# Performance work log

Measured on AMD Instinct MI355X. Metric: run time of the kernel, lower is better.

## Reference

```python
import jax, jax.numpy as jnp
import numpy as np

# Dimensions: batch B, window W (time features), nodes M, hidden HID, hops NLAYERS
B, W, M, HID, NLAYERS = 32, 168, 2048, 128, 6


def setup_inputs() -> dict:
    key = jax.random.key(0)
    ks = jax.random.split(key, 6)
    x = jax.random.normal(ks[0], (B, W, M), dtype=jnp.float32)
    # scale L so matrix powers L^k stay bounded (spectral radius < 1)
    L = jax.random.normal(ks[1], (M, M), dtype=jnp.float32) / (2.0 * np.float32(np.sqrt(M)))
    # stacked per-hop MLP params: linears[i]: W->HID, linears2[i]: HID->1
    W1 = jax.random.normal(ks[2], (NLAYERS + 1, HID, W), dtype=jnp.float32) / np.float32(np.sqrt(W))
    b1 = jax.random.normal(ks[3], (NLAYERS + 1, HID), dtype=jnp.float32) * 0.01
    W2 = jax.random.normal(ks[4], (NLAYERS + 1, HID), dtype=jnp.float32) / np.float32(np.sqrt(HID))
    b2 = jax.random.normal(ks[5], (NLAYERS + 1,), dtype=jnp.float32) * 0.01
    return {"x": x, "L": L, "W1": W1, "b1": b1, "W2": W2, "b2": b2}


def _hop_mlp(t, w1, bb1, w2, bb2):
    # t: [B, M, W] -> scalar score per node: Linear(W->HID), ReLU, Linear(HID->1)
    h = jax.nn.relu(jnp.einsum('bmw,hw->bmh', t, w1) + bb1)
    return jnp.einsum('bmh,h->bm', h, w2) + bb2


def reference(x, L, W1, b1, W2, b2):
    xt = jnp.swapaxes(x, 1, 2)  # [B, M, W] (x.transpose(2,1))
    s = _hop_mlp(xt, W1[0], b1[0], W2[0], b2[0])  # [B, M]
    P = L
    for i in range(1, NLAYERS + 1):
        # PP.expand + bmm == broadcasted matmul; never materialize [B,M,M]
        t = jnp.einsum('ij,bjw->biw', P, xt)  # [B, M, W]
        s = s + _hop_mlp(t, W1[i], b1[i], W2[i], b2[i])
        P = jnp.matmul(L, P)  # next graph power
    return s  # [B, M]; output_fun is None so no final nonlinearity
```

## Files before the change

kernel.cpp:

```cpp
#include <hip/hip_runtime.h>
#include <cstdint>
#include <cstddef>

typedef __bf16 bf16_t;
typedef __attribute__((ext_vector_type(8))) __bf16 bf16x8;
typedef __attribute__((ext_vector_type(4))) __bf16 bf16x4;
typedef __attribute__((ext_vector_type(4))) float floatx4;

#define NB 32
#define NW 168
#define NM 2048
#define NHID 128
#define NBW (NB * NW)
#define NGEMM 168
#define NMLPB 256

#define GLOAD_LDS16(g, l)                                          \
  __builtin_amdgcn_global_load_lds(                                \
      (const __attribute__((address_space(1))) void*)(g),          \
      (__attribute__((address_space(3))) void*)(l), 16, 0, 0)

__global__ void cast_bf16_kernel(const float* __restrict__ in, bf16_t* __restrict__ out, int n4) {
  int stride = gridDim.x * blockDim.x;
  for (int i = blockIdx.x * blockDim.x + threadIdx.x; i < n4; i += stride) {
    float4 v = ((const float4*)in)[i];
    bf16x4 o = {(bf16_t)v.x, (bf16_t)v.y, (bf16_t)v.z, (bf16_t)v.w};
    ((bf16x4*)out)[i] = o;
  }
}

__global__ void prep_x_kernel(const float* __restrict__ x, bf16_t* __restrict__ Xb,
                              bf16_t* __restrict__ XT) {
  __shared__ float tile[64][65];
  const int R = NBW, C = NM;
  int r0 = blockIdx.y * 64, c0 = blockIdx.x * 64;
  int t = threadIdx.x;
  int tr = t >> 4, tc4 = (t & 15) * 4;
#pragma unroll
  for (int p = 0; p < 4; ++p) {
    int row = p * 16 + tr;
    float4 v = *(const float4*)(x + (size_t)(r0 + row) * C + c0 + tc4);
    tile[row][tc4 + 0] = v.x;
    tile[row][tc4 + 1] = v.y;
    tile[row][tc4 + 2] = v.z;
    tile[row][tc4 + 3] = v.w;
    bf16x4 o = {(bf16_t)v.x, (bf16_t)v.y, (bf16_t)v.z, (bf16_t)v.w};
    *(bf16x4*)(Xb + (size_t)(r0 + row) * C + c0 + tc4) = o;
  }
  __syncthreads();
#pragma unroll
  for (int p = 0; p < 4; ++p) {
    int c = p * 16 + tr;
    bf16x4 o = {(bf16_t)tile[tc4 + 0][c], (bf16_t)tile[tc4 + 1][c],
                (bf16_t)tile[tc4 + 2][c], (bf16_t)tile[tc4 + 3][c]};
    *(bf16x4*)(XT + (size_t)(c0 + c) * R + r0 + tc4) = o;
  }
}

__device__ __forceinline__ void mlp_half(
    int t2, int r0, bf16_t* __restrict__ Bs, float* __restrict__ sred,
    const bf16_t* __restrict__ T, const bf16_t* __restrict__ Wh,
    const float* __restrict__ b1h, const float* __restrict__ w2h, float b2v,
    float* __restrict__ out, int accumulate) {
  int lane = t2 & 63, wvh = t2 >> 6;
  int wm = wvh >> 1, wn = wvh & 1;
  int quad = lane >> 4, l15 = lane & 15;

  for (int c = 2688 + t2; c < 3072; c += 256) {
    int4 z = {0, 0, 0, 0};
    *(int4*)(Bs + (size_t)c * 8) = z;
  }
  for (int i = 0; i < 11; ++i) {
    int c = i * 256 + t2;
    if (c < 2688) {
      int kc = c >> 7;
      int h = (c & 127) ^ ((kc & 3) << 2);
      GLOAD_LDS16(Wh + (size_t)h * NW + kc * 8, Bs + (size_t)(i * 256 + wvh * 64) * 8);
    }
  }

  const bf16_t* arow[4];
#pragma unroll
  for (int mi = 0; mi < 4; ++mi) {
    int R = r0 + wm * 64 + mi * 16 + l15;
    arow[mi] = T + (size_t)(R >> 5) * NBW + (size_t)(R & 31) * NW + quad * 8;
  }

  floatx4 zero4 = {0.f, 0.f, 0.f, 0.f};
  floatx4 acc[4][4];
#pragma unroll
  for (int mi = 0; mi < 4; ++mi)
#pragma unroll
    for (int ni = 0; ni < 4; ++ni) acc[mi][ni] = zero4;

  __syncthreads();

#pragma unroll
  for (int kb = 0; kb < 192; kb += 32) {
    int kc = (kb >> 3) + quad;
    bf16x8 af[4], bf[4];
#pragma unroll
    for (int mi = 0; mi < 4; ++mi)
      af[mi] = *(const bf16x8*)(arow[mi] + kb);
#pragma unroll
    for (int ni = 0; ni < 4; ++ni) {
      int hpos = (wn * 64 + ni * 16 + l15) ^ ((kc & 3) << 2);
      bf[ni] = *(const bf16x8*)(Bs + (size_t)(kc * 128 + hpos) * 8);
    }
#pragma unroll
    for (int mi = 0; mi < 4; ++mi)
#pragma unroll
      for (int ni = 0; ni < 4; ++ni)
        acc[mi][ni] = __builtin_amdgcn_mfma_f32_16x16x32_bf16(af[mi], bf[ni], acc[mi][ni], 0, 0, 0);
  }

  float part[4][4];
#pragma unroll
  for (int mi = 0; mi < 4; ++mi)
#pragma unroll
    for (int r = 0; r < 4; ++r) part[mi][r] = 0.f;
#pragma unroll
  for (int ni = 0; ni < 4; ++ni) {
    int col = wn * 64 + ni * 16 + l15;
    float b1v = b1h[col];
    float w2v = w2h[col];
#pragma unroll
    for (int mi = 0; mi < 4; ++mi)
#pragma unroll
      for (int r = 0; r < 4; ++r) {
        float h = acc[mi][ni][r] + b1v;
        h = h > 0.f ? h : 0.f;
        part[mi][r] += h * w2v;
      }
  }
#pragma unroll
  for (int off = 1; off < 16; off <<= 1)
#pragma unroll
    for (int mi = 0; mi < 4; ++mi)
#pragma unroll
      for (int r = 0; r < 4; ++r) part[mi][r] += __shfl_xor(part[mi][r], off);
  if (l15 == 0) {
#pragma unroll
    for (int mi = 0; mi < 4; ++mi)
#pragma unroll
      for (int r = 0; r < 4; ++r) sred[wvh * 64 + mi * 16 + quad * 4 + r] = part[mi][r];
  }
  __syncthreads();
  if (t2 < 128) {
    int hh = t2 >> 6;
    int lr = t2 & 63;
    float v = sred[(hh * 2) * 64 + lr] + sred[(hh * 2 + 1) * 64 + lr] + b2v;
    int R = r0 + hh * 64 + lr;
    int idx = (R & 31) * NM + (R >> 5);
    if (accumulate)
      out[idx] += v;
    else
      out[idx] = v;
  }
}

#define STAGE2(gbase, ld, t, ks, ldsbase)                                        \
  do {                                                                           \
    const bf16_t* _g = (gbase) + (size_t)(t) * 64 + (ks) * 32;                   \
    GLOAD_LDS16(_g, lds + (ldsbase) + (ks) * 8192 + wv * 512);                   \
    GLOAD_LDS16(_g + (size_t)128 * (ld),                                         \
                lds + (ldsbase) + (ks) * 8192 + 4096 + wv * 512);                \
  } while (0)

#define VM4 asm volatile("s_waitcnt vmcnt(4)" ::: "memory")

#define PHASE(bufoff, ks, mh, READB, STG, WAIT)                                  \
  do {                                                                           \
    if (READB) {                                                                 \
      _Pragma("unroll") for (int ni = 0; ni < 4; ++ni)                           \
          bfr[ni] = *(const bf16x8*)(pB + (bufoff) + (ks) * 8192 + ni * 512);    \
    }                                                                            \
    _Pragma("unroll") for (int mi = 0; mi < 4; ++mi)                             \
        afr[mi] =                                                                \
            *(const bf16x8*)(pA + (bufoff) + (ks) * 8192 + ((mh) * 4 + mi) * 512); \
    __builtin_amdgcn_s_barrier();                                                \
    asm volatile("s_waitcnt lgkmcnt(0)" ::: "memory");                           \
    __builtin_amdgcn_s_setprio(1);                                               \
    _Pragma("unroll") for (int mi = 0; mi < 4; ++mi)                             \
        _Pragma("unroll") for (int ni = 0; ni < 4; ++ni)                         \
            acc[(mh) * 4 + mi][ni] = __builtin_amdgcn_mfma_f32_16x16x32_bf16(    \
                afr[mi], bfr[ni], acc[(mh) * 4 + mi][ni], 0, 0, 0);              \
    __builtin_amdgcn_s_setprio(0);                                               \
    STG;                                                                         \
    WAIT;                                                                        \
    __builtin_amdgcn_s_barrier();                                                \
  } while (0)

__global__ __launch_bounds__(512, 2) void fused_gemm_mlp_kernel(
    const bf16_t* __restrict__ A, const bf16_t* __restrict__ Bt,
    bf16_t* __restrict__ C, bf16_t* __restrict__ Ct,
    int K, int lda, int ldb, int ldc, int ldct, int write_c,
    const bf16_t* __restrict__ T, const bf16_t* __restrict__ W1b,
    const float* __restrict__ b1, const float* __restrict__ W2,
    const float* __restrict__ b2, float* __restrict__ out,
    int hop, int accumulate) {
  __shared__ bf16_t lds[65536];
  const int bx = blockIdx.x;
  const int tid = threadIdx.x;

  if (bx >= NGEMM) {
    int j = bx - NGEMM;
    int h = tid >> 8;
    int t2 = tid & 255;
    bf16_t* Bs = lds + (size_t)h * 24576;
    float* sred = (float*)(lds + 49152) + h * 256;
    int r0 = (2 * j + h) * 128;
    mlp_half(t2, r0, Bs, sred, T, W1b + (size_t)hop * NHID * NW,
             b1 + hop * NHID, W2 + hop * NHID, b2[hop], out, accumulate);
    return;
  }

  const int m0 = (bx >> 3) * 256, n0 = (bx & 7) * 256;
  const int lane = tid & 63, wv = tid >> 6;
  const int wm = wv >> 2, wn = wv & 3;
  const int quad = lane >> 4, l15 = lane & 15;

  const int srow = tid >> 2;
  const int scsw = (tid & 3) ^ ((srow >> 1) & 3);
  const bf16_t* aS = A + (size_t)(m0 + srow) * lda + scsw * 8;
  const bf16_t* bS = Bt + (size_t)(n0 + srow) * ldb + scsw * 8;

  const int fsw = (quad ^ ((l15 >> 1) & 3)) * 8;
  const bf16_t* pA = lds + (size_t)(wm * 128 + l15) * 32 + fsw;
  const bf16_t* pB = lds + 16384 + (size_t)(wn * 64 + l15) * 32 + fsw;

  floatx4 zero4 = {0.f, 0.f, 0.f, 0.f};
  floatx4 acc[8][4];
#pragma unroll
  for (int mi = 0; mi < 8; ++mi)
#pragma unroll
    for (int ni = 0; ni < 4; ++ni) acc[mi][ni] = zero4;

  STAGE2(aS, lda, 0, 0, 0);
  STAGE2(bS, ldb, 0, 0, 16384);
  STAGE2(aS, lda, 0, 1, 0);
  STAGE2(bS, ldb, 0, 1, 16384);
  STAGE2(aS, lda, 1, 0, 32768);
  STAGE2(bS, ldb, 1, 0, 49152);
  VM4;
  __builtin_amdgcn_s_barrier();

  bf16x8 afr[4], bfr[4];
  const int nt = K >> 6;
  const int nit = K >> 7;
#pragma unroll 1
  for (int i = 0; i < nit; ++i) {
    const int t1 = 2 * i + 1;
    const int t2 = (t1 + 1 < nt) ? t1 + 1 : 0;
    const int t3 = (t1 + 2 < nt) ? t1 + 2 : 0;
    PHASE(0,     0, 0, 1, STAGE2(aS, lda, t1, 1, 32768), (void)0);
    PHASE(0,     0, 1, 0, STAGE2(bS, ldb, t1, 1, 49152), (void)0);
    PHASE(0,     1, 0, 1, STAGE2(aS, lda, t2, 0, 0),     (void)0);
    PHASE(0,     1, 1, 0, STAGE2(bS, ldb, t2, 0, 16384), VM4);
    PHASE(32768, 0, 0, 1, STAGE2(aS, lda, t2, 1, 0),     (void)0);
    PHASE(32768, 0, 1, 0, STAGE2(bS, ldb, t2, 1, 16384), (void)0);
    PHASE(32768, 1, 0, 1, STAGE2(aS, lda, t3, 0, 32768), (void)0);
    PHASE(32768, 1, 1, 0, STAGE2(bS, ldb, t3, 0, 49152), VM4);
  }
  asm volatile("s_waitcnt vmcnt(0)" ::: "memory");

#pragma unroll
  for (int mi = 0; mi < 8; ++mi) {
#pragma unroll
    for (int ni = 0; ni < 4; ++ni) {
      int col = n0 + wn * 64 + ni * 16 + l15;
      int rowb = m0 + wm * 128 + mi * 16 + quad * 4;
      bf16x4 tv;
#pragma unroll
      for (int r = 0; r < 4; ++r) tv[r] = (bf16_t)acc[mi][ni][r];
      *(bf16x4*)(Ct + (size_t)col * ldct + rowb) = tv;
      if (write_c) {
#pragma unroll
        for (int r = 0; r < 4; ++r)
          C[(size_t)(rowb + r) * ldc + col] = tv[r];
      }
    }
  }
}

__global__ void mlp_score_kernel(const bf16_t* __restrict__ T, const bf16_t* __restrict__ W1b,
                                 const float* __restrict__ b1, const float* __restrict__ W2,
                                 const float* __restrict__ b2, float* __restrict__ out,
                                 int hop, int accumulate) {
  __shared__ bf16_t Bs[24 * 128 * 8];
  __shared__ float sred[256];
  mlp_half(threadIdx.x, blockIdx.x * 128, Bs, sred, T,
           W1b + (size_t)hop * NHID * NW, b1 + hop * NHID, W2 + hop * NHID,
           b2[hop], out, accumulate);
}

extern "C" void kernel_launch(void* const* d_in, const int* in_sizes, int n_in,
                              void* d_out, int out_size, void* d_ws, size_t ws_size,
                              hipStream_t stream) {
  const float* x = (const float*)d_in[0];
  const float* L = (const float*)d_in[1];
  const float* W1 = (const float*)d_in[2];
  const float* b1 = (const float*)d_in[3];
  const float* W2 = (const float*)d_in[4];
  const float* b2 = (const float*)d_in[5];
  float* out = (float*)d_out;

  char* ws = (char*)d_ws;
  size_t off = 0;
  auto walloc = [&](size_t bytes) -> void* {
    off = (off + 255) & ~(size_t)255;
    void* p = ws + off;
    off += bytes;
    return p;
  };
  bf16_t* Xb = (bf16_t*)walloc((size_t)NBW * NM * 2);
  bf16_t* XT0 = (bf16_t*)walloc((size_t)NM * NBW * 2);
  bf16_t* XT1 = (bf16_t*)walloc((size_t)NM * NBW * 2);
  bf16_t* Lb = (bf16_t*)walloc((size_t)NM * NM * 2);
  bf16_t* W1b = (bf16_t*)walloc((size_t)7 * NHID * NW * 2);
  bf16_t* Ta = (bf16_t*)walloc((size_t)NBW * NM * 2);
  (void)ws_size; (void)in_sizes; (void)n_in; (void)out_size;

  prep_x_kernel<<<dim3(NM / 64, NBW / 64), dim3(256), 0, stream>>>(x, Xb, XT0);
  cast_bf16_kernel<<<dim3(1024), dim3(256), 0, stream>>>(L, Lb, NM * NM / 4);
  cast_bf16_kernel<<<dim3(64), dim3(256), 0, stream>>>(W1, W1b, 7 * NHID * NW / 4);

  bf16_t* src = Xb;
  bf16_t* dst = Ta;
  bf16_t* xtprev = XT0;
  bf16_t* xtcur = XT1;
  for (int i = 1; i <= 6; ++i) {
    fused_gemm_mlp_kernel<<<dim3(NGEMM + NMLPB), dim3(512), 0, stream>>>(
        src, Lb, dst, xtcur, NM, NM, NM, NM, NBW, (i < 6) ? 1 : 0,
        xtprev, W1b, b1, W2, b2, out, i - 1, (i > 1) ? 1 : 0);
    bf16_t* t = src; src = dst; dst = t;
    t = xtprev; xtprev = xtcur; xtcur = t;
  }
  mlp_score_kernel<<<dim3(NM * NB / 128), dim3(256), 0, stream>>>(
      xtprev, W1b, b1, W2, b2, out, 6, 1);
}
```

Measured before the change: 473.6 us.

## Double-buffer LDS fragment reads in GEMM loop and split MLP blocks

The GEMM main loop now reads the next A/B fragments from LDS into a second register set before issuing the current MFMAs. This replaces the read-barrier-wait-compute phases with a software-pipelined schedule that has fewer full barriers and a looser vmcnt wait. The MLP side of the fused kernel changes from two 128-row halves per 512-thread block to one 128-row tile per block, doubling the MLP block count. In those blocks only 256 threads compute, which may waste occupancy, and the extra fragment registers add register pressure.

```diff
diff --git a/kernel.cpp b/kernel.cpp
--- a/kernel.cpp
+++ b/kernel.cpp
@@ -13,7 +13,7 @@
 #define NHID 128
 #define NBW (NB * NW)
 #define NGEMM 168
-#define NMLPB 256
+#define NMLPB 512
 
 #define GLOAD_LDS16(g, l)                                          \
   __builtin_amdgcn_global_load_lds(                                \
@@ -57,98 +57,99 @@
   }
 }
 
-__device__ __forceinline__ void mlp_half(
-    int t2, int r0, bf16_t* __restrict__ Bs, float* __restrict__ sred,
+__device__ __forceinline__ void mlp_single(
+    int tid, int r0, bf16_t* __restrict__ Bs,
     const bf16_t* __restrict__ T, const bf16_t* __restrict__ Wh,
     const float* __restrict__ b1h, const float* __restrict__ w2h, float b2v,
     float* __restrict__ out, int accumulate) {
-  int lane = t2 & 63, wvh = t2 >> 6;
-  int wm = wvh >> 1, wn = wvh & 1;
-  int quad = lane >> 4, l15 = lane & 15;
-
-  for (int c = 2688 + t2; c < 3072; c += 256) {
-    int4 z = {0, 0, 0, 0};
-    *(int4*)(Bs + (size_t)c * 8) = z;
-  }
-  for (int i = 0; i < 11; ++i) {
-    int c = i * 256 + t2;
-    if (c < 2688) {
+  float* sred = (float*)(Bs + 24576);
+  int lane = tid & 63, wv2 = tid >> 6;
+
+#pragma unroll
+  for (int i = 0; i < 6; ++i) {
+    int c = i * 512 + tid;
+    if (c >= 2688) {
+      int4 z = {0, 0, 0, 0};
+      *(int4*)(Bs + (size_t)c * 8) = z;
+    } else {
       int kc = c >> 7;
       int h = (c & 127) ^ ((kc & 3) << 2);
-      GLOAD_LDS16(Wh + (size_t)h * NW + kc * 8, Bs + (size_t)(i * 256 + wvh * 64) * 8);
-    }
-  }
-
-  const bf16_t* arow[4];
-#pragma unroll
-  for (int mi = 0; mi < 4; ++mi) {
-    int R = r0 + wm * 64 + mi * 16 + l15;
-    arow[mi] = T + (size_t)(R >> 5) * NBW + (size_t)(R & 31) * NW + quad * 8;
-  }
-
-  floatx4 zero4 = {0.f, 0.f, 0.f, 0.f};
-  floatx4 acc[4][4];
-#pragma unroll
-  for (int mi = 0; mi < 4; ++mi)
-#pragma unroll
-    for (int ni = 0; ni < 4; ++ni) acc[mi][ni] = zero4;
-
+      GLOAD_LDS16(Wh + (size_t)h * NW + kc * 8, Bs + (size_t)(i * 512 + wv2 * 64) * 8);
+    }
+  }
   __syncthreads();
 
-#pragma unroll
-  for (int kb = 0; kb < 192; kb += 32) {
-    int kc = (kb >> 3) + quad;
-    bf16x8 af[4], bf[4];
+  if (tid < 256) {
+    int wm = wv2 >> 1, wn = wv2 & 1;
+    int quad = lane >> 4, l15 = lane & 15;
+    const bf16_t* arow[4];
+#pragma unroll
+    for (int mi = 0; mi < 4; ++mi) {
+      int R = r0 + wm * 64 + mi * 16 + l15;
+      arow[mi] = T + (size_t)(R >> 5) * NBW + (size_t)(R & 31) * NW + quad * 8;
+    }
+    floatx4 zero4 = {0.f, 0.f, 0.f, 0.f};
+    floatx4 acc[4][4];
 #pragma unroll
     for (int mi = 0; mi < 4; ++mi)
-      af[mi] = *(const bf16x8*)(arow[mi] + kb);
+#pragma unroll
+      for (int ni = 0; ni < 4; ++ni) acc[mi][ni] = zero4;
+
+#pragma unroll
+    for (int kb = 0; kb < 192; kb += 32) {
+      int kc = (kb >> 3) + quad;
+      bf16x8 af[4], bf[4];
+#pragma unroll
+      for (int mi = 0; mi < 4; ++mi)
+        af[mi] = *(const bf16x8*)(arow[mi] + kb);
+#pragma unroll
+      for (int ni = 0; ni < 4; ++ni) {
+        int hpos = (wn * 64 + ni * 16 + l15) ^ ((kc & 3) << 2);
+        bf[ni] = *(const bf16x8*)(Bs + (size_t)(kc * 128 + hpos) * 8);
+      }
+#pragma unroll
+      for (int mi = 0; mi < 4; ++mi)
+#pragma unroll
+        for (int ni = 0; ni < 4; ++ni)
+          acc[mi][ni] = __builtin_amdgcn_mfma_f32_16x16x32_bf16(af[mi], bf[ni], acc[mi][ni], 0, 0, 0);
+    }
+
+    float part[4][4];
+#pragma unroll
+    for (int mi = 0; mi < 4; ++mi)
+#pragma unroll
+      for (int r = 0; r < 4; ++r) part[mi][r] = 0.f;
 #pragma unroll
     for (int ni = 0; ni < 4; ++ni) {
-      int hpos = (wn * 64 + ni * 16 + l15) ^ ((kc & 3) << 2);
-      bf[ni] = *(const bf16x8*)(Bs + (size_t)(kc * 128 + hpos) * 8);
-    }
-#pragma unroll
-    for (int mi = 0; mi < 4; ++mi)
-#pragma unroll
-      for (int ni = 0; ni < 4; ++ni)
-        acc[mi][ni] = __builtin_amdgcn_mfma_f32_16x16x32_bf16(af[mi], bf[ni], acc[mi][ni], 0, 0, 0);
-  }
-
-  float part[4][4];
-#pragma unroll
-  for (int mi = 0; mi < 4; ++mi)
-#pragma unroll
-    for (int r = 0; r < 4; ++r) part[mi][r] = 0.f;
-#pragma unroll
-  for (int ni = 0; ni < 4; ++ni) {
-    int col = wn * 64 + ni * 16 + l15;
-    float b1v = b1h[col];
-    float w2v = w2h[col];
-#pragma unroll
-    for (int mi = 0; mi < 4; ++mi)
-#pragma unroll
-      for (int r = 0; r < 4; ++r) {
-        float h = acc[mi][ni][r] + b1v;
-        h = h > 0.f ? h : 0.f;
-        part[mi][r] += h * w2v;
-      }
-  }
-#pragma unroll
-  for (int off = 1; off < 16; off <<= 1)
-#pragma unroll
-    for (int mi = 0; mi < 4; ++mi)
-#pragma unroll
-      for (int r = 0; r < 4; ++r) part[mi][r] += __shfl_xor(part[mi][r], off);
-  if (l15 == 0) {
-#pragma unroll
-    for (int mi = 0; mi < 4; ++mi)
-#pragma unroll
-      for (int r = 0; r < 4; ++r) sred[wvh * 64 + mi * 16 + quad * 4 + r] = part[mi][r];
+      int col = wn * 64 + ni * 16 + l15;
+      float b1v = b1h[col];
+      float w2v = w2h[col];
+#pragma unroll
+      for (int mi = 0; mi < 4; ++mi)
+#pragma unroll
+        for (int r = 0; r < 4; ++r) {
+          float h = acc[mi][ni][r] + b1v;
+          h = h > 0.f ? h : 0.f;
+          part[mi][r] += h * w2v;
+        }
+    }
+#pragma unroll
+    for (int off = 1; off < 16; off <<= 1)
+#pragma unroll
+      for (int mi = 0; mi < 4; ++mi)
+#pragma unroll
+        for (int r = 0; r < 4; ++r) part[mi][r] += __shfl_xor(part[mi][r], off);
+    if (l15 == 0) {
+#pragma unroll
+      for (int mi = 0; mi < 4; ++mi)
+#pragma unroll
+        for (int r = 0; r < 4; ++r) sred[wv2 * 64 + mi * 16 + quad * 4 + r] = part[mi][r];
+    }
   }
   __syncthreads();
-  if (t2 < 128) {
-    int hh = t2 >> 6;
-    int lr = t2 & 63;
+  if (tid < 128) {
+    int hh = tid >> 6;
+    int lr = tid & 63;
     float v = sred[(hh * 2) * 64 + lr] + sred[(hh * 2 + 1) * 64 + lr] + b2v;
     int R = r0 + hh * 64 + lr;
     int idx = (R & 31) * NM + (R >> 5);
@@ -167,28 +168,26 @@
                 lds + (ldsbase) + (ks) * 8192 + 4096 + wv * 512);                \
   } while (0)
 
-#define VM4 asm volatile("s_waitcnt vmcnt(4)" ::: "memory")
-
-#define PHASE(bufoff, ks, mh, READB, STG, WAIT)                                  \
+#define VM6 asm volatile("s_waitcnt vmcnt(6)" ::: "memory")
+#define TOPB asm volatile("s_barrier" ::: "memory")
+#define ENDB __builtin_amdgcn_s_barrier()
+
+#define RD_A(dst, bufoff, ks, mh)                                                \
+  _Pragma("unroll") for (int mi = 0; mi < 4; ++mi)                               \
+      dst[mi] = *(const bf16x8*)(pA + (bufoff) + (ks) * 8192 + ((mh) * 4 + mi) * 512)
+
+#define RD_B(dst, bufoff, ks)                                                    \
+  _Pragma("unroll") for (int ni = 0; ni < 4; ++ni)                               \
+      dst[ni] = *(const bf16x8*)(pB + (bufoff) + (ks) * 8192 + ni * 512)
+
+#define MM16(af_, bf_, mh)                                                       \
   do {                                                                           \
-    if (READB) {                                                                 \
-      _Pragma("unroll") for (int ni = 0; ni < 4; ++ni)                           \
-          bfr[ni] = *(const bf16x8*)(pB + (bufoff) + (ks) * 8192 + ni * 512);    \
-    }                                                                            \
-    _Pragma("unroll") for (int mi = 0; mi < 4; ++mi)                             \
-        afr[mi] =                                                                \
-            *(const bf16x8*)(pA + (bufoff) + (ks) * 8192 + ((mh) * 4 + mi) * 512); \
-    __builtin_amdgcn_s_barrier();                                                \
-    asm volatile("s_waitcnt lgkmcnt(0)" ::: "memory");                           \
     __builtin_amdgcn_s_setprio(1);                                               \
     _Pragma("unroll") for (int mi = 0; mi < 4; ++mi)                             \
         _Pragma("unroll") for (int ni = 0; ni < 4; ++ni)                         \
             acc[(mh) * 4 + mi][ni] = __builtin_amdgcn_mfma_f32_16x16x32_bf16(    \
-                afr[mi], bfr[ni], acc[(mh) * 4 + mi][ni], 0, 0, 0);              \
+                af_[mi], bf_[ni], acc[(mh) * 4 + mi][ni], 0, 0, 0);              \
     __builtin_amdgcn_s_setprio(0);                                               \
-    STG;                                                                         \
-    WAIT;                                                                        \
-    __builtin_amdgcn_s_barrier();                                                \
   } while (0)
 
 __global__ __launch_bounds__(512, 2) void fused_gemm_mlp_kernel(
@@ -205,13 +204,8 @@
 
   if (bx >= NGEMM) {
     int j = bx - NGEMM;
-    int h = tid >> 8;
-    int t2 = tid & 255;
-    bf16_t* Bs = lds + (size_t)h * 24576;
-    float* sred = (float*)(lds + 49152) + h * 256;
-    int r0 = (2 * j + h) * 128;
-    mlp_half(t2, r0, Bs, sred, T, W1b + (size_t)hop * NHID * NW,
-             b1 + hop * NHID, W2 + hop * NHID, b2[hop], out, accumulate);
+    mlp_single(tid, j * 128, lds, T, W1b + (size_t)hop * NHID * NW,
+               b1 + hop * NHID, W2 + hop * NHID, b2[hop], out, accumulate);
     return;
   }
 
@@ -242,10 +236,13 @@
   STAGE2(bS, ldb, 0, 1, 16384);
   STAGE2(aS, lda, 1, 0, 32768);
   STAGE2(bS, ldb, 1, 0, 49152);
-  VM4;
-  __builtin_amdgcn_s_barrier();
-
-  bf16x8 afr[4], bfr[4];
+  asm volatile("s_waitcnt vmcnt(8)" ::: "memory");
+  TOPB;
+
+  bf16x8 af0[4], af1[4], bf0[4], bf1[4];
+  RD_B(bf0, 0, 0);
+  RD_A(af0, 0, 0, 0);
+
   const int nt = K >> 6;
   const int nit = K >> 7;
 #pragma unroll 1
@@ -253,14 +250,46 @@
     const int t1 = 2 * i + 1;
     const int t2 = (t1 + 1 < nt) ? t1 + 1 : 0;
     const int t3 = (t1 + 2 < nt) ? t1 + 2 : 0;
-    PHASE(0,     0, 0, 1, STAGE2(aS, lda, t1, 1, 32768), (void)0);
-    PHASE(0,     0, 1, 0, STAGE2(bS, ldb, t1, 1, 49152), (void)0);
-    PHASE(0,     1, 0, 1, STAGE2(aS, lda, t2, 0, 0),     (void)0);
-    PHASE(0,     1, 1, 0, STAGE2(bS, ldb, t2, 0, 16384), VM4);
-    PHASE(32768, 0, 0, 1, STAGE2(aS, lda, t2, 1, 0),     (void)0);
-    PHASE(32768, 0, 1, 0, STAGE2(bS, ldb, t2, 1, 16384), (void)0);
-    PHASE(32768, 1, 0, 1, STAGE2(aS, lda, t3, 0, 32768), (void)0);
-    PHASE(32768, 1, 1, 0, STAGE2(bS, ldb, t3, 0, 49152), VM4);
+    RD_A(af1, 0, 0, 1);
+    MM16(af0, bf0, 0);
+    STAGE2(aS, lda, t1, 1, 32768);
+    ENDB;
+    VM6; TOPB;
+    RD_B(bf1, 0, 1);
+    RD_A(af0, 0, 1, 0);
+    MM16(af1, bf0, 1);
+    STAGE2(bS, ldb, t1, 1, 49152);
+    ENDB;
+    RD_A(af1, 0, 1, 1);
+    MM16(af0, bf1, 0);
+    STAGE2(aS, lda, t2, 0, 0);
+    ENDB;
+    VM6; TOPB;
+    RD_B(bf0, 32768, 0);
+    RD_A(af0, 32768, 0, 0);
+    MM16(af1, bf1, 1);
+    STAGE2(bS, ldb, t2, 0, 16384);
+    ENDB;
+    RD_A(af1, 32768, 0, 1);
+    MM16(af0, bf0, 0);
+    STAGE2(aS, lda, t2, 1, 0);
+    ENDB;
+    VM6; TOPB;
+    RD_B(bf1, 32768, 1);
+    RD_A(af0, 32768, 1, 0);
+    MM16(af1, bf0, 1);
+    STAGE2(bS, ldb, t2, 1, 16384);
+    ENDB;
+    RD_A(af1, 32768, 1, 1);
+    MM16(af0, bf1, 0);
+    STAGE2(aS, lda, t3, 0, 32768);
+    ENDB;
+    VM6; TOPB;
+    RD_B(bf0, 0, 0);
+    RD_A(af0, 0, 0, 0);
+    MM16(af1, bf1, 1);
+    STAGE2(bS, ldb, t3, 0, 49152);
+    ENDB;
   }
   asm volatile("s_waitcnt vmcnt(0)" ::: "memory");
 
@@ -283,15 +312,15 @@
   }
 }
 
-__global__ void mlp_score_kernel(const bf16_t* __restrict__ T, const bf16_t* __restrict__ W1b,
-                                 const float* __restrict__ b1, const float* __restrict__ W2,
-                                 const float* __restrict__ b2, float* __restrict__ out,
-                                 int hop, int accumulate) {
-  __shared__ bf16_t Bs[24 * 128 * 8];
-  __shared__ float sred[256];
-  mlp_half(threadIdx.x, blockIdx.x * 128, Bs, sred, T,
-           W1b + (size_t)hop * NHID * NW, b1 + hop * NHID, W2 + hop * NHID,
-           b2[hop], out, accumulate);
+__global__ __launch_bounds__(512) void mlp_score_kernel(
+    const bf16_t* __restrict__ T, const bf16_t* __restrict__ W1b,
+    const float* __restrict__ b1, const float* __restrict__ W2,
+    const float* __restrict__ b2, float* __restrict__ out,
+    int hop, int accumulate) {
+  __shared__ bf16_t Bs[24 * 128 * 8 + 512];
+  mlp_single(threadIdx.x, blockIdx.x * 128, Bs, T,
+             W1b + (size_t)hop * NHID * NW, b1 + hop * NHID, W2 + hop * NHID,
+             b2[hop], out, accumulate);
 }
 
 extern "C" void kernel_launch(void* const* d_in, const int* in_sizes, int n_in,
@@ -336,6 +365,6 @@
     bf16_t* t = src; src = dst; dst = t;
     t = xtprev; xtprev = xtcur; xtcur = t;
   }
-  mlp_score_kernel<<<dim3(NM * NB / 128), dim3(256), 0, stream>>>(
+  mlp_score_kernel<<<dim3(NM * NB / 128), dim3(512), 0, stream>>>(
       xtprev, W1b, b1, W2, b2, out, 6, 1);
 }
```

Result: no change. 466.0 us (-1.6%).

## Shrink GEMM tiles to 128x128 with triple-buffered K=32 pipeline and higher occupancy

Applied to the files above, without the earlier changes.

The GEMM tile drops from 256x256 to 128x128 and the grid grows from 168 to 672 GEMM blocks, launched in a swizzled order. The old 8-phase double-buffered K=64 schedule is replaced by a simple 3-stage ring of K=32 LDS buffers, cutting LDS to about 50KB and targeting 4 blocks per CU. The MLP part now runs one 512-thread block per 256 rows, and the final score kernel is launched the same way. The aim is better CU fill and latency hiding from more concurrent blocks. The cost is less data reuse per tile, so global and L2 traffic goes up.

```diff
diff --git a/kernel.cpp b/kernel.cpp
--- a/kernel.cpp
+++ b/kernel.cpp
@@ -12,7 +12,7 @@
 #define NM 2048
 #define NHID 128
 #define NBW (NB * NW)
-#define NGEMM 168
+#define NGEMM 672
 #define NMLPB 256
 
 #define GLOAD_LDS16(g, l)                                          \
@@ -57,100 +57,101 @@
   }
 }
 
-__device__ __forceinline__ void mlp_half(
-    int t2, int r0, bf16_t* __restrict__ Bs, float* __restrict__ sred,
+__device__ __forceinline__ void mlp_block(
+    int tid, int r0, bf16_t* __restrict__ Bs,
     const bf16_t* __restrict__ T, const bf16_t* __restrict__ Wh,
     const float* __restrict__ b1h, const float* __restrict__ w2h, float b2v,
     float* __restrict__ out, int accumulate) {
-  int lane = t2 & 63, wvh = t2 >> 6;
-  int wm = wvh >> 1, wn = wvh & 1;
-  int quad = lane >> 4, l15 = lane & 15;
-
-  for (int c = 2688 + t2; c < 3072; c += 256) {
-    int4 z = {0, 0, 0, 0};
-    *(int4*)(Bs + (size_t)c * 8) = z;
-  }
-  for (int i = 0; i < 11; ++i) {
-    int c = i * 256 + t2;
-    if (c < 2688) {
+  float* sred = (float*)(Bs + 24576);
+  int lane = tid & 63, wv2 = tid >> 6;
+
+#pragma unroll
+  for (int i = 0; i < 6; ++i) {
+    int c = i * 512 + tid;
+    if (c >= 2688) {
+      int4 z = {0, 0, 0, 0};
+      *(int4*)(Bs + (size_t)c * 8) = z;
+    } else {
       int kc = c >> 7;
       int h = (c & 127) ^ ((kc & 3) << 2);
-      GLOAD_LDS16(Wh + (size_t)h * NW + kc * 8, Bs + (size_t)(i * 256 + wvh * 64) * 8);
-    }
-  }
-
-  const bf16_t* arow[4];
-#pragma unroll
-  for (int mi = 0; mi < 4; ++mi) {
-    int R = r0 + wm * 64 + mi * 16 + l15;
-    arow[mi] = T + (size_t)(R >> 5) * NBW + (size_t)(R & 31) * NW + quad * 8;
-  }
-
-  floatx4 zero4 = {0.f, 0.f, 0.f, 0.f};
-  floatx4 acc[4][4];
-#pragma unroll
-  for (int mi = 0; mi < 4; ++mi)
-#pragma unroll
-    for (int ni = 0; ni < 4; ++ni) acc[mi][ni] = zero4;
-
+      GLOAD_LDS16(Wh + (size_t)h * NW + kc * 8, Bs + (size_t)(i * 512 + wv2 * 64) * 8);
+    }
+  }
   __syncthreads();
 
-#pragma unroll
-  for (int kb = 0; kb < 192; kb += 32) {
-    int kc = (kb >> 3) + quad;
-    bf16x8 af[4], bf[4];
+  {
+    int wm = wv2 >> 1, wn = wv2 & 1;
+    int quad = lane >> 4, l15 = lane & 15;
+    const bf16_t* arow[4];
+#pragma unroll
+    for (int mi = 0; mi < 4; ++mi) {
+      int R = r0 + wm * 64 + mi * 16 + l15;
+      arow[mi] = T + (size_t)(R >> 5) * NBW + (size_t)(R & 31) * NW + quad * 8;
+    }
+    floatx4 zero4 = {0.f, 0.f, 0.f, 0.f};
+    floatx4 acc[4][4];
 #pragma unroll
     for (int mi = 0; mi < 4; ++mi)
-      af[mi] = *(const bf16x8*)(arow[mi] + kb);
+#pragma unroll
+      for (int ni = 0; ni < 4; ++ni) acc[mi][ni] = zero4;
+
+#pragma unroll
+    for (int kb = 0; kb < 192; kb += 32) {
+      int kc = (kb >> 3) + quad;
+      bf16x8 af[4], bf[4];
+#pragma unroll
+      for (int mi = 0; mi < 4; ++mi)
+        af[mi] = *(const bf16x8*)(arow[mi] + kb);
+#pragma unroll
+      for (int ni = 0; ni < 4; ++ni) {
+        int hpos = (wn * 64 + ni * 16 + l15) ^ ((kc & 3) << 2);
+        bf[ni] = *(const bf16x8*)(Bs + (size_t)(kc * 128 + hpos) * 8);
+      }
+#pragma unroll
+      for (int mi = 0; mi < 4; ++mi)
+#pragma unroll
+        for (int ni = 0; ni < 4; ++ni)
+          acc[mi][ni] = __builtin_amdgcn_mfma_f32_16x16x32_bf16(af[mi], bf[ni], acc[mi][ni], 0, 0, 0);
+    }
+
+    float part[4][4];
+#pragma unroll
+    for (int mi = 0; mi < 4; ++mi)
+#pragma unroll
+      for (int r = 0; r < 4; ++r) part[mi][r] = 0.f;
 #pragma unroll
     for (int ni = 0; ni < 4; ++ni) {
-      int hpos = (wn * 64 + ni * 16 + l15) ^ ((kc & 3) << 2);
-      bf[ni] = *(const bf16x8*)(Bs + (size_t)(kc * 128 + hpos) * 8);
-    }
-#pragma unroll
-    for (int mi = 0; mi < 4; ++mi)
-#pragma unroll
-      for (int ni = 0; ni < 4; ++ni)
-        acc[mi][ni] = __builtin_amdgcn_mfma_f32_16x16x32_bf16(af[mi], bf[ni], acc[mi][ni], 0, 0, 0);
-  }
-
-  float part[4][4];
-#pragma unroll
-  for (int mi = 0; mi < 4; ++mi)
-#pragma unroll
-    for (int r = 0; r < 4; ++r) part[mi][r] = 0.f;
-#pragma unroll
-  for (int ni = 0; ni < 4; ++ni) {
-    int col = wn * 64 + ni * 16 + l15;
-    float b1v = b1h[col];
-    float w2v = w2h[col];
-#pragma unroll
-    for (int mi = 0; mi < 4; ++mi)
-#pragma unroll
-      for (int r = 0; r < 4; ++r) {
-        float h = acc[mi][ni][r] + b1v;
-        h = h > 0.f ? h : 0.f;
-        part[mi][r] += h * w2v;
-      }
-  }
-#pragma unroll
-  for (int off = 1; off < 16; off <<= 1)
-#pragma unroll
-    for (int mi = 0; mi < 4; ++mi)
-#pragma unroll
-      for (int r = 0; r < 4; ++r) part[mi][r] += __shfl_xor(part[mi][r], off);
-  if (l15 == 0) {
-#pragma unroll
-    for (int mi = 0; mi < 4; ++mi)
-#pragma unroll
-      for (int r = 0; r < 4; ++r) sred[wvh * 64 + mi * 16 + quad * 4 + r] = part[mi][r];
+      int col = wn * 64 + ni * 16 + l15;
+      float b1v = b1h[col];
+      float w2v = w2h[col];
+#pragma unroll
+      for (int mi = 0; mi < 4; ++mi)
+#pragma unroll
+        for (int r = 0; r < 4; ++r) {
+          float h = acc[mi][ni][r] + b1v;
+          h = h > 0.f ? h : 0.f;
+          part[mi][r] += h * w2v;
+        }
+    }
+#pragma unroll
+    for (int off = 1; off < 16; off <<= 1)
+#pragma unroll
+      for (int mi = 0; mi < 4; ++mi)
+#pragma unroll
+        for (int r = 0; r < 4; ++r) part[mi][r] += __shfl_xor(part[mi][r], off);
+    if (l15 == 0) {
+#pragma unroll
+      for (int mi = 0; mi < 4; ++mi)
+#pragma unroll
+        for (int r = 0; r < 4; ++r) sred[wv2 * 64 + mi * 16 + quad * 4 + r] = part[mi][r];
+    }
   }
   __syncthreads();
-  if (t2 < 128) {
-    int hh = t2 >> 6;
-    int lr = t2 & 63;
-    float v = sred[(hh * 2) * 64 + lr] + sred[(hh * 2 + 1) * 64 + lr] + b2v;
-    int R = r0 + hh * 64 + lr;
+  if (tid < 256) {
+    int wm = tid >> 6;
+    int lr = tid & 63;
+    float v = sred[(wm * 2) * 64 + lr] + sred[(wm * 2 + 1) * 64 + lr] + b2v;
+    int R = r0 + wm * 64 + lr;
     int idx = (R & 31) * NM + (R >> 5);
     if (accumulate)
       out[idx] += v;
@@ -159,39 +160,13 @@
   }
 }
 
-#define STAGE2(gbase, ld, t, ks, ldsbase)                                        \
-  do {                                                                           \
-    const bf16_t* _g = (gbase) + (size_t)(t) * 64 + (ks) * 32;                   \
-    GLOAD_LDS16(_g, lds + (ldsbase) + (ks) * 8192 + wv * 512);                   \
-    GLOAD_LDS16(_g + (size_t)128 * (ld),                                         \
-                lds + (ldsbase) + (ks) * 8192 + 4096 + wv * 512);                \
+#define STG(c_, t_)                                                          \
+  do {                                                                       \
+    GLOAD_LDS16(aS + (size_t)(t_) * 32, lds + (c_) * 8192 + wv * 512);       \
+    GLOAD_LDS16(bS + (size_t)(t_) * 32, lds + (c_) * 8192 + 4096 + wv * 512);\
   } while (0)
 
-#define VM4 asm volatile("s_waitcnt vmcnt(4)" ::: "memory")
-
-#define PHASE(bufoff, ks, mh, READB, STG, WAIT)                                  \
-  do {                                                                           \
-    if (READB) {                                                                 \
-      _Pragma("unroll") for (int ni = 0; ni < 4; ++ni)                           \
-          bfr[ni] = *(const bf16x8*)(pB + (bufoff) + (ks) * 8192 + ni * 512);    \
-    }                                                                            \
-    _Pragma("unroll") for (int mi = 0; mi < 4; ++mi)                             \
-        afr[mi] =                                                                \
-            *(const bf16x8*)(pA + (bufoff) + (ks) * 8192 + ((mh) * 4 + mi) * 512); \
-    __builtin_amdgcn_s_barrier();                                                \
-    asm volatile("s_waitcnt lgkmcnt(0)" ::: "memory");                           \
-    __builtin_amdgcn_s_setprio(1);                                               \
-    _Pragma("unroll") for (int mi = 0; mi < 4; ++mi)                             \
-        _Pragma("unroll") for (int ni = 0; ni < 4; ++ni)                         \
-            acc[(mh) * 4 + mi][ni] = __builtin_amdgcn_mfma_f32_16x16x32_bf16(    \
-                afr[mi], bfr[ni], acc[(mh) * 4 + mi][ni], 0, 0, 0);              \
-    __builtin_amdgcn_s_setprio(0);                                               \
-    STG;                                                                         \
-    WAIT;                                                                        \
-    __builtin_amdgcn_s_barrier();                                                \
-  } while (0)
-
-__global__ __launch_bounds__(512, 2) void fused_gemm_mlp_kernel(
+__global__ __launch_bounds__(512, 4) void fused_gemm_mlp_kernel(
     const bf16_t* __restrict__ A, const bf16_t* __restrict__ Bt,
     bf16_t* __restrict__ C, bf16_t* __restrict__ Ct,
     int K, int lda, int ldb, int ldc, int ldct, int write_c,
@@ -199,23 +174,19 @@
     const float* __restrict__ b1, const float* __restrict__ W2,
     const float* __restrict__ b2, float* __restrict__ out,
     int hop, int accumulate) {
-  __shared__ bf16_t lds[65536];
+  __shared__ bf16_t lds[25600];
   const int bx = blockIdx.x;
   const int tid = threadIdx.x;
 
   if (bx >= NGEMM) {
     int j = bx - NGEMM;
-    int h = tid >> 8;
-    int t2 = tid & 255;
-    bf16_t* Bs = lds + (size_t)h * 24576;
-    float* sred = (float*)(lds + 49152) + h * 256;
-    int r0 = (2 * j + h) * 128;
-    mlp_half(t2, r0, Bs, sred, T, W1b + (size_t)hop * NHID * NW,
-             b1 + hop * NHID, W2 + hop * NHID, b2[hop], out, accumulate);
+    mlp_block(tid, j * 256, lds, T, W1b + (size_t)hop * NHID * NW,
+              b1 + hop * NHID, W2 + hop * NHID, b2[hop], out, accumulate);
     return;
   }
 
-  const int m0 = (bx >> 3) * 256, n0 = (bx & 7) * 256;
+  const int sid = (bx & 7) * 84 + (bx >> 3);
+  const int m0 = (sid >> 4) * 128, n0 = (sid & 15) * 128;
   const int lane = tid & 63, wv = tid >> 6;
   const int wm = wv >> 2, wn = wv & 3;
   const int quad = lane >> 4, l15 = lane & 15;
@@ -226,50 +197,54 @@
   const bf16_t* bS = Bt + (size_t)(n0 + srow) * ldb + scsw * 8;
 
   const int fsw = (quad ^ ((l15 >> 1) & 3)) * 8;
-  const bf16_t* pA = lds + (size_t)(wm * 128 + l15) * 32 + fsw;
-  const bf16_t* pB = lds + 16384 + (size_t)(wn * 64 + l15) * 32 + fsw;
 
   floatx4 zero4 = {0.f, 0.f, 0.f, 0.f};
-  floatx4 acc[8][4];
-#pragma unroll
-  for (int mi = 0; mi < 8; ++mi)
-#pragma unroll
-    for (int ni = 0; ni < 4; ++ni) acc[mi][ni] = zero4;
-
-  STAGE2(aS, lda, 0, 0, 0);
-  STAGE2(bS, ldb, 0, 0, 16384);
-  STAGE2(aS, lda, 0, 1, 0);
-  STAGE2(bS, ldb, 0, 1, 16384);
-  STAGE2(aS, lda, 1, 0, 32768);
-  STAGE2(bS, ldb, 1, 0, 49152);
-  VM4;
+  floatx4 acc[4][2];
+#pragma unroll
+  for (int mi = 0; mi < 4; ++mi)
+#pragma unroll
+    for (int ni = 0; ni < 2; ++ni) acc[mi][ni] = zero4;
+
+  STG(0, 0);
+  STG(1, 1);
+  asm volatile("s_waitcnt vmcnt(2)" ::: "memory");
   __builtin_amdgcn_s_barrier();
 
-  bf16x8 afr[4], bfr[4];
-  const int nt = K >> 6;
-  const int nit = K >> 7;
+  const int nk = K >> 5;
+  int c = 0;
 #pragma unroll 1
-  for (int i = 0; i < nit; ++i) {
-    const int t1 = 2 * i + 1;
-    const int t2 = (t1 + 1 < nt) ? t1 + 1 : 0;
-    const int t3 = (t1 + 2 < nt) ? t1 + 2 : 0;
-    PHASE(0,     0, 0, 1, STAGE2(aS, lda, t1, 1, 32768), (void)0);
-    PHASE(0,     0, 1, 0, STAGE2(bS, ldb, t1, 1, 49152), (void)0);
-    PHASE(0,     1, 0, 1, STAGE2(aS, lda, t2, 0, 0),     (void)0);
-    PHASE(0,     1, 1, 0, STAGE2(bS, ldb, t2, 0, 16384), VM4);
-    PHASE(32768, 0, 0, 1, STAGE2(aS, lda, t2, 1, 0),     (void)0);
-    PHASE(32768, 0, 1, 0, STAGE2(bS, ldb, t2, 1, 16384), (void)0);
-    PHASE(32768, 1, 0, 1, STAGE2(aS, lda, t3, 0, 32768), (void)0);
-    PHASE(32768, 1, 1, 0, STAGE2(bS, ldb, t3, 0, 49152), VM4);
+  for (int t = 0; t < nk; ++t) {
+    int tt = (t + 2 < nk) ? t + 2 : 0;
+    int cn = c + 2; if (cn >= 3) cn -= 3;
+    STG(cn, tt);
+    const bf16_t* pa = lds + c * 8192;
+    const bf16_t* pb = pa + 4096;
+    bf16x8 af[4], bf[2];
+#pragma unroll
+    for (int ni = 0; ni < 2; ++ni)
+      bf[ni] = *(const bf16x8*)(pb + (wn * 32 + ni * 16 + l15) * 32 + fsw);
+#pragma unroll
+    for (int mi = 0; mi < 4; ++mi)
+      af[mi] = *(const bf16x8*)(pa + (wm * 64 + mi * 16 + l15) * 32 + fsw);
+    __builtin_amdgcn_s_setprio(1);
+#pragma unroll
+    for (int mi = 0; mi < 4; ++mi)
+#pragma unroll
+      for (int ni = 0; ni < 2; ++ni)
+        acc[mi][ni] = __builtin_amdgcn_mfma_f32_16x16x32_bf16(af[mi], bf[ni], acc[mi][ni], 0, 0, 0);
+    __builtin_amdgcn_s_setprio(0);
+    asm volatile("s_waitcnt vmcnt(2)" ::: "memory");
+    __builtin_amdgcn_s_barrier();
+    c = (c + 1 == 3) ? 0 : c + 1;
   }
   asm volatile("s_waitcnt vmcnt(0)" ::: "memory");
 
 #pragma unroll
-  for (int mi = 0; mi < 8; ++mi) {
-#pragma unroll
-    for (int ni = 0; ni < 4; ++ni) {
-      int col = n0 + wn * 64 + ni * 16 + l15;
-      int rowb = m0 + wm * 128 + mi * 16 + quad * 4;
+  for (int mi = 0; mi < 4; ++mi) {
+#pragma unroll
+    for (int ni = 0; ni < 2; ++ni) {
+      int col = n0 + wn * 32 + ni * 16 + l15;
+      int rowb = m0 + wm * 64 + mi * 16 + quad * 4;
       bf16x4 tv;
 #pragma unroll
       for (int r = 0; r < 4; ++r) tv[r] = (bf16_t)acc[mi][ni][r];
@@ -283,15 +258,15 @@
   }
 }
 
-__global__ void mlp_score_kernel(const bf16_t* __restrict__ T, const bf16_t* __restrict__ W1b,
-                                 const float* __restrict__ b1, const float* __restrict__ W2,
-                                 const float* __restrict__ b2, float* __restrict__ out,
-                                 int hop, int accumulate) {
-  __shared__ bf16_t Bs[24 * 128 * 8];
-  __shared__ float sred[256];
-  mlp_half(threadIdx.x, blockIdx.x * 128, Bs, sred, T,
-           W1b + (size_t)hop * NHID * NW, b1 + hop * NHID, W2 + hop * NHID,
-           b2[hop], out, accumulate);
+__global__ __launch_bounds__(512, 4) void mlp_score_kernel(
+    const bf16_t* __restrict__ T, const bf16_t* __restrict__ W1b,
+    const float* __restrict__ b1, const float* __restrict__ W2,
+    const float* __restrict__ b2, float* __restrict__ out,
+    int hop, int accumulate) {
+  __shared__ bf16_t Bs[25600];
+  mlp_block(threadIdx.x, blockIdx.x * 256, Bs, T,
+            W1b + (size_t)hop * NHID * NW, b1 + hop * NHID, W2 + hop * NHID,
+            b2[hop], out, accumulate);
 }
 
 extern "C" void kernel_launch(void* const* d_in, const int* in_sizes, int n_in,
@@ -336,6 +311,6 @@
     bf16_t* t = src; src = dst; dst = t;
     t = xtprev; xtprev = xtcur; xtcur = t;
   }
-  mlp_score_kernel<<<dim3(NM * NB / 128), dim3(256), 0, stream>>>(
+  mlp_score_kernel<<<dim3(NM * NB / 256), dim3(512), 0, stream>>>(
       xtprev, W1b, b1, W2, b2, out, 6, 1);
 }
```

Result: slower. 543.7 us (+14.8%).
